# Kernel optimization log

Hardware: AMD Instinct MI355X
Metric: run time of the kernel (lower is better)

## Reference

```python
import jax, jax.numpy as jnp
import numpy as np

EPS = 1e-7
R = 3  # routing iterations


def conv(x, k, b, stride):
    y = jax.lax.conv_general_dilated(x, k, (stride, stride), 'VALID',
                                     dimension_numbers=('NHWC', 'HWIO', 'NHWC'))
    return y + b


def squash(s):
    n = jnp.linalg.norm(s, axis=-1, keepdims=True)
    return (n * n) / (1.0 + n * n) * s / (n + EPS)


def setup_inputs() -> dict:
    key = jax.random.key(0)
    ks = jax.random.split(key, 12)
    B = 256

    def g(k, shape, scale=0.05):
        return jax.random.normal(k, shape, dtype=jnp.float32) * scale

    return dict(
        x=jax.random.normal(ks[0], (B, 40, 40, 1), dtype=jnp.float32),
        y=jax.random.randint(ks[1], (B,), 0, 10),
        conv1_k=g(ks[2], (5, 5, 1, 64)),   conv1_b=jnp.zeros((64,), jnp.float32),
        conv2_k=g(ks[3], (9, 9, 64, 128)), conv2_b=jnp.zeros((128,), jnp.float32),
        conv3_k=g(ks[4], (9, 9, 128, 256)), conv3_b=jnp.zeros((256,), jnp.float32),
        prim_k=g(ks[5], (9, 9, 256, 256)), prim_b=jnp.zeros((256,), jnp.float32),
        w=g(ks[6], (1152, 10, 16, 8)),
        d1_w=g(ks[7], (160, 1024)),  d1_b=jnp.zeros((1024,), jnp.float32),
        d2_w=g(ks[8], (1024, 2048)), d2_b=jnp.zeros((2048,), jnp.float32),
        d3_w=g(ks[9], (2048, 1600)), d3_b=jnp.zeros((1600,), jnp.float32),
    )


def reference(x, y, conv1_k, conv1_b, conv2_k, conv2_b, conv3_k, conv3_b,
              prim_k, prim_b, w, d1_w, d1_b, d2_w, d2_b, d3_w, d3_b):
    # conv stack: 40 -> 36 -> 28 -> 20 -> 6 (primary caps, stride 2, linear)
    h = jax.nn.relu(conv(x, conv1_k, conv1_b, 1))
    h = jax.nn.relu(conv(h, conv2_k, conv2_b, 1))
    h = jax.nn.relu(conv(h, conv3_k, conv3_b, 1))
    h = conv(h, prim_k, prim_b, 2)                      # [B,6,6,256]
    B = h.shape[0]
    u = h.reshape(B, 1152, 8)                           # 1152 primary capsules of dim 8

    # pose predictions: u_hat[b,i,j,k] = sum_v w[i,j,k,v] * u[b,i,v]
    u_hat = jnp.einsum('ijkv,biv->bijk', w, u)          # [B,1152,10,16]

    # dynamic routing by agreement
    b_logit = jnp.zeros((B, 1152, 10), dtype=u_hat.dtype)
    for _ in range(R):
        c = jax.nn.softmax(b_logit, axis=2)[..., None]          # [B,1152,10,1]
        s = jnp.sum(c * u_hat, axis=1, keepdims=True)           # [B,1,10,16]
        v = squash(s)                                           # [B,1,10,16]
        b_logit = b_logit + jnp.sum(u_hat * v, axis=-1)         # agreement

    # masking by true label and reconstruction
    yh = jax.nn.one_hot(y, 10, dtype=v.dtype)                   # [B,10]
    v_masked = yh[:, None, :, None] * v                         # [B,1,10,16]
    v_flat = v_masked.reshape(B, 10 * 16)
    r1 = jax.nn.relu(v_flat @ d1_w + d1_b)
    r2 = jax.nn.relu(r1 @ d2_w + d2_b)
    recon = jax.nn.sigmoid(r2 @ d3_w + d3_b)                    # [B,1600]
    return (v, recon)
```

## Files before the change

kernel.cpp:

```cpp
#include <hip/hip_runtime.h>
#include <hip/hip_bf16.h>

typedef _Float16 f16;
typedef __attribute__((ext_vector_type(8))) _Float16 f16x8;
typedef __attribute__((ext_vector_type(4))) float f32x4;

__device__ __forceinline__ void gload_lds16(const void* g, void* l) {
  __builtin_amdgcn_global_load_lds((const __attribute__((address_space(1))) void*)g,
                                   (__attribute__((address_space(3))) void*)l, 16, 0, 0);
}

template<int CIN, int COUT>
__global__ __launch_bounds__(256) void wtrans_kernel(const float* __restrict__ src,
                                                     f16* __restrict__ dst) {
  constexpr int KT = 81 * CIN;
  __shared__ float tile[64][65];
  int k0 = blockIdx.x * 64;
  int n0 = blockIdx.y * 64;
  int t = threadIdx.x;
#pragma unroll
  for (int i = 0; i < 16; ++i) {
    int id = t + i * 256;
    int r = id >> 6, c = id & 63;
    tile[r][c] = src[(k0 + r) * COUT + n0 + c];
  }
  __syncthreads();
#pragma unroll
  for (int i = 0; i < 16; ++i) {
    int id = t + i * 256;
    int r = id >> 6, c = id & 63;
    dst[(n0 + r) * KT + k0 + c] = (f16)tile[c][r];
  }
}

__global__ __launch_bounds__(256) void wtransg_kernel(const float* __restrict__ src,
                                                      f16* __restrict__ dst,
                                                      int K, int N, int NP) {
  __shared__ float tile[64][65];
  int k0 = blockIdx.x * 64;
  int n0 = blockIdx.y * 64;
  int t = threadIdx.x;
#pragma unroll
  for (int i = 0; i < 16; ++i) {
    int id = t + i * 256;
    int r = id >> 6, c = id & 63;
    tile[r][c] = (n0 + c < N) ? src[(k0 + r) * N + n0 + c] : 0.f;
  }
  __syncthreads();
#pragma unroll
  for (int i = 0; i < 16; ++i) {
    int id = t + i * 256;
    int r = id >> 6, c = id & 63;
    dst[(size_t)(n0 + r) * K + k0 + c] = (f16)tile[c][r];
  }
}

__global__ __launch_bounds__(256) void cvtf16_kernel(const float* __restrict__ src,
                                                     f16* __restrict__ dst, int n) {
  int idx = blockIdx.x * 256 + threadIdx.x;
  if (idx < n) dst[idx] = (f16)src[idx];
}

__global__ __launch_bounds__(256) void conv1_kernel(const float* __restrict__ x,
                                                    const float* __restrict__ kw,
                                                    const float* __restrict__ bias,
                                                    f16* __restrict__ out) {
  int idx = blockIdx.x * 256 + threadIdx.x;
  int g = idx & 7;
  int co0 = g * 8;
  int r = idx >> 3;
  int ow = r % 36; int r2 = r / 36; int oh = r2 % 36; int b = r2 / 36;
  float acc[8];
#pragma unroll
  for (int j = 0; j < 8; ++j) acc[j] = bias[co0 + j];
  const float* xp = x + (b * 40 + oh) * 40 + ow;
#pragma unroll
  for (int dy = 0; dy < 5; ++dy)
#pragma unroll
    for (int dx = 0; dx < 5; ++dx) {
      float xv = xp[dy * 40 + dx];
      const float* kp = kw + (dy * 5 + dx) * 64 + co0;
#pragma unroll
      for (int j = 0; j < 8; ++j) acc[j] += xv * kp[j];
    }
  f16x8 o;
#pragma unroll
  for (int j = 0; j < 8; ++j) o[j] = (f16)fmaxf(acc[j], 0.f);
  *(f16x8*)(out + r * 64 + co0) = o;
}

template<int CIN, int WIN>
__device__ __forceinline__ int tapA_off(int kt) {
  int tap, ci0;
  if (CIN == 64)       { tap = kt;      ci0 = 0; }
  else if (CIN == 128) { tap = kt >> 1; ci0 = (kt & 1) << 6; }
  else                 { tap = kt >> 2; ci0 = (kt & 3) << 6; }
  int dy = tap / 9, dx = tap - dy * 9;
  return (dy * WIN + dx) * CIN + ci0;
}

template<int HIN, int WIN, int CIN, int HOUT, int WOUT, int COUT, int STRIDE,
         bool RELU, bool OUTF16>
__global__ __launch_bounds__(512, 2) void conv8p_kernel(const f16* __restrict__ in,
                                                        const f16* __restrict__ wt,
                                                        const float* __restrict__ bias,
                                                        f16* __restrict__ out16,
                                                        float* __restrict__ out32) {
  static_assert(COUT == 256, "BN=256 template requires COUT==256");
  constexpr int KTOT = 81 * CIN;
  constexpr int NT = KTOT / 64;
  __shared__ __align__(16) f16 lds[65536];
  const int mb = (int)blockIdx.x;
  const int t = threadIdx.x;
  const int wave = t >> 6, lane = t & 63;
  const int hi = lane >> 4, lo = lane & 15;
  const int wm = wave >> 2, wn = wave & 3;

  int Aoff[4], Boff[4];
  {
    int g = (lane & 7) ^ ((lane >> 3) & 7);
#pragma unroll
    for (int rbi = 0; rbi < 4; ++rbi) {
      int r = rbi * 64 + 8 * wave + (lane >> 3);
      int m = mb * 256 + r;
      int b = m / (HOUT * WOUT);
      int rr = m - b * (HOUT * WOUT);
      int oh = rr / WOUT, ow = rr - oh * WOUT;
      Aoff[rbi] = ((b * HIN + oh * STRIDE) * WIN + ow * STRIDE) * CIN + g * 8;
      Boff[rbi] = r * KTOT + g * 8;
    }
  }
  const int gb0 = (hi ^ (lo & 7)) << 4;
  const int gb1 = ((4 + hi) ^ (lo & 7)) << 4;

  const char* ldsc = (const char*)lds;
  char* ldsw = (char*)lds;

#define GA(rbi, tpo, bq) gload_lds16(in + Aoff[rbi] + (tpo),                        \
    (void*)(ldsw + (bq) * 32768 + ((rbi) * 64 + 8 * wave) * 128))
#define GB(rbi, tile) gload_lds16(wt + Boff[rbi] + ((tile) << 6),                   \
    (void*)(ldsw + 65536 + ((tile) & 1) * 32768 + ((rbi) * 64 + 8 * wave) * 128))

  {
    int tp0 = tapA_off<CIN, WIN>(0);
    GA(0, tp0, 0); GA(2, tp0, 0); GA(1, tp0, 0); GA(3, tp0, 0);
    GB(0, 0); GB(1, 0); GB(2, 0); GB(3, 0);
    GB(0, 1); GB(1, 1); GB(2, 1); GB(3, 1);
    asm volatile("s_waitcnt vmcnt(4)" ::: "memory");
    __builtin_amdgcn_s_barrier();
  }

  f32x4 acc[8][4] = {};

#define DO_PHASE(Q, STAGE)                                                          \
  {                                                                                 \
    f16x8 af[2][2];                                                                 \
    _Pragma("unroll")                                                               \
    for (int mf = 0; mf < 2; ++mf) {                                                \
      af[mf][0] = *(const f16x8*)(Ab + ((Q) * 2 + mf) * 2048 + gb0);                \
      af[mf][1] = *(const f16x8*)(Ab + ((Q) * 2 + mf) * 2048 + gb1);                \
    }                                                                               \
    STAGE;                                                                          \
    __builtin_amdgcn_s_barrier();                                                   \
    asm volatile("s_waitcnt lgkmcnt(0)" ::: "memory");                              \
    __builtin_amdgcn_sched_barrier(0);                                              \
    __builtin_amdgcn_s_setprio(1);                                                  \
    _Pragma("unroll")                                                               \
    for (int sb = 0; sb < 2; ++sb)                                                  \
      _Pragma("unroll")                                                             \
      for (int mf = 0; mf < 2; ++mf)                                                \
        _Pragma("unroll")                                                           \
        for (int nf = 0; nf < 4; ++nf)                                              \
          acc[(Q) * 2 + mf][nf] = __builtin_amdgcn_mfma_f32_16x16x32_f16(           \
              af[mf][sb], bfr[nf][sb], acc[(Q) * 2 + mf][nf], 0, 0, 0);             \
    __builtin_amdgcn_s_setprio(0);                                                  \
    __builtin_amdgcn_s_barrier();                                                   \
  }

  for (int T = 0; T < NT; ++T) {
    const int q = T & 1;
    const char* Ab = ldsc + q * 32768 + wm * 16384 + lo * 128;
    const char* Bb = ldsc + 65536 + q * 32768 + wn * 8192 + lo * 128;
    const int tpn = tapA_off<CIN, WIN>(T + 1);
    f16x8 bfr[4][2];
#pragma unroll
    for (int nf = 0; nf < 4; ++nf) {
      bfr[nf][0] = *(const f16x8*)(Bb + nf * 2048 + gb0);
      bfr[nf][1] = *(const f16x8*)(Bb + nf * 2048 + gb1);
    }
    DO_PHASE(0, if (T + 1 < NT) { GA(0, tpn, (T + 1) & 1); GA(2, tpn, (T + 1) & 1); })
    DO_PHASE(1, if (T + 1 < NT) { GA(1, tpn, (T + 1) & 1); GA(3, tpn, (T + 1) & 1); })
    DO_PHASE(2, if (T + 2 < NT) { GB(0, T + 2); GB(1, T + 2); })
    DO_PHASE(3,
      if (T + 2 < NT) {
        GB(2, T + 2); GB(3, T + 2);
        asm volatile("s_waitcnt vmcnt(4)" ::: "memory");
      } else {
        asm volatile("s_waitcnt vmcnt(0)" ::: "memory");
      })
  }
#undef DO_PHASE
#undef GA
#undef GB

#pragma unroll
  for (int mfr = 0; mfr < 8; ++mfr) {
#pragma unroll
    for (int nf = 0; nf < 4; ++nf) {
      int m0 = mb * 256 + wm * 128 + mfr * 16 + hi * 4;
      int n = wn * 64 + nf * 16 + lo;
      float bval = bias[n];
#pragma unroll
      for (int r = 0; r < 4; ++r) {
        float v = acc[mfr][nf][r] + bval;
        if (RELU) v = fmaxf(v, 0.f);
        int o = (m0 + r) * COUT + n;
        if (OUTF16) out16[o] = (f16)v; else out32[o] = v;
      }
    }
  }
}

template<int HIN, int WIN, int CIN, int HOUT, int WOUT, int COUT, int STRIDE,
         bool RELU, bool OUTF16, int SPLIT, bool ADDBIAS>
__global__ __launch_bounds__(256) void conv_mfma_kernel(const f16* __restrict__ in,
                                                        const f16* __restrict__ wt,
                                                        const float* __restrict__ bias,
                                                        f16* __restrict__ out16,
                                                        float* __restrict__ out32) {
  constexpr int KTOT = 81 * CIN;
  constexpr int NBLK = COUT / 128;
  constexpr int MTOT = 256 * HOUT * WOUT;
  constexpr int MBNB = (MTOT / 128) * NBLK;
  constexpr int NKT = (KTOT / 64) / SPLIT;
  __shared__ __align__(16) f16 lds[16384];
  int bidx = (int)blockIdx.x;
  int ks = 0;
  if (SPLIT > 1) { ks = bidx / MBNB; bidx -= ks * MBNB; }
  const int mb = bidx / NBLK;
  const int nb = bidx % NBLK;
  const int t = threadIdx.x;
  const int wave = t >> 6, lane = t & 63;
  const int hi = lane >> 4, lo = lane & 15;
  const bool isA = wave < 2;
  const int slot0 = wave << 9;

  int baseoff[8];
#pragma unroll
  for (int it = 0; it < 8; ++it) {
    int s = slot0 + it * 64 + lane;
    if (isA) {
      int row = s >> 3;
      int g = (s & 7) ^ (row & 7);
      int mg = mb * 128 + row;
      int b = mg / (HOUT * WOUT);
      int rr = mg - b * (HOUT * WOUT);
      int oh = rr / WOUT;
      int ow = rr - oh * WOUT;
      baseoff[it] = ((b * HIN + oh * STRIDE) * WIN + ow * STRIDE) * CIN + g * 8;
    } else {
      int sl = s - 1024;
      int row = sl >> 3;
      int g = (sl & 7) ^ (row & 7);
      baseoff[it] = (nb * 128 + row) * KTOT + g * 8;
    }
  }
  const f16* gsrc = isA ? in : wt;

  int aQ[4], bQ[4];
  const int wm = wave >> 1, wn = wave & 1;
#pragma unroll
  for (int f = 0; f < 4; ++f) {
    int arow = wm * 64 + f * 16 + lo;
    aQ[f] = (arow * 128) ^ ((arow & 7) << 4);
    int brow = wn * 64 + f * 16 + lo;
    bQ[f] = 16384 + ((brow * 128) ^ ((brow & 7) << 4));
  }

  f32x4 acc[4][4] = {};
  const char* ldsc = (const char*)lds;

  const int kt0 = ks * NKT;
  for (int kt = kt0; kt < kt0 + NKT; ++kt) {
    int tapoff;
    if (isA) tapoff = tapA_off<CIN, WIN>(kt);
    else     tapoff = kt << 6;
    __syncthreads();
#pragma unroll
    for (int it = 0; it < 8; ++it)
      gload_lds16(gsrc + baseoff[it] + tapoff,
                  (void*)((char*)lds + ((slot0 + it * 64) << 4)));
    __syncthreads();
#pragma unroll
    for (int sub = 0; sub < 2; ++sub) {
      const int gx = (sub * 4 + hi) << 4;
      f16x8 av[4], bv[4];
#pragma unroll
      for (int f = 0; f < 4; ++f) av[f] = *(const f16x8*)(ldsc + (aQ[f] ^ gx));
#pragma unroll
      for (int f = 0; f < 4; ++f) bv[f] = *(const f16x8*)(ldsc + (bQ[f] ^ gx));
#pragma unroll
      for (int mf = 0; mf < 4; ++mf)
#pragma unroll
        for (int nf = 0; nf < 4; ++nf)
          acc[mf][nf] = __builtin_amdgcn_mfma_f32_16x16x32_f16(av[mf], bv[nf],
                                                               acc[mf][nf], 0, 0, 0);
    }
  }

  float* o32 = out32 + (size_t)ks * MTOT * COUT;
#pragma unroll
  for (int mf = 0; mf < 4; ++mf) {
#pragma unroll
    for (int nf = 0; nf < 4; ++nf) {
      int m0 = mb * 128 + wm * 64 + mf * 16 + hi * 4;
      int n = nb * 128 + wn * 64 + nf * 16 + lo;
      float bval = ADDBIAS ? bias[n] : 0.f;
#pragma unroll
      for (int r = 0; r < 4; ++r) {
        float v = acc[mf][nf][r] + bval;
        if (RELU) v = fmaxf(v, 0.f);
        int o = (m0 + r) * COUT + n;
        if (OUTF16) out16[o] = (f16)v; else o32[o] = v;
      }
    }
  }
}

__global__ __launch_bounds__(256) void prim_reduce_kernel(const float* __restrict__ part,
                                                          const float* __restrict__ bias,
                                                          float* __restrict__ p) {
  int idx = blockIdx.x * 256 + threadIdx.x;
  int n = idx & 255;
  float a = bias[n];
#pragma unroll
  for (int s = 0; s < 4; ++s) a += part[s * 2359296 + idx];
  p[idx] = a;
}

template<int K, int NP, int NOUT, int ACT>
__global__ __launch_bounds__(256) void gemm_mfma_kernel(const f16* __restrict__ A,
                                                        const f16* __restrict__ Bw,
                                                        const float* __restrict__ bias,
                                                        f16* __restrict__ out16,
                                                        float* __restrict__ out32) {
  constexpr int NBLK = NP / 128;
  __shared__ __align__(16) f16 lds[16384];
  const int mb = (int)blockIdx.x / NBLK;
  const int nb = (int)blockIdx.x % NBLK;
  const int t = threadIdx.x;
  const int wave = t >> 6, lane = t & 63;
  const int hi = lane >> 4, lo = lane & 15;
  const bool isA = wave < 2;
  const int slot0 = wave << 9;

  int baseoff[8];
#pragma unroll
  for (int it = 0; it < 8; ++it) {
    int s = slot0 + it * 64 + lane;
    if (isA) {
      int row = s >> 3;
      int g = (s & 7) ^ (row & 7);
      baseoff[it] = (mb * 128 + row) * K + g * 8;
    } else {
      int sl = s - 1024;
      int row = sl >> 3;
      int g = (sl & 7) ^ (row & 7);
      baseoff[it] = (nb * 128 + row) * K + g * 8;
    }
  }
  const f16* gsrc = isA ? A : Bw;

  int aQ[4], bQ[4];
  const int wm = wave >> 1, wn = wave & 1;
#pragma unroll
  for (int f = 0; f < 4; ++f) {
    int arow = wm * 64 + f * 16 + lo;
    aQ[f] = (arow * 128) ^ ((arow & 7) << 4);
    int brow = wn * 64 + f * 16 + lo;
    bQ[f] = 16384 + ((brow * 128) ^ ((brow & 7) << 4));
  }

  f32x4 acc[4][4] = {};
  const char* ldsc = (const char*)lds;

  for (int kt = 0; kt < K / 64; ++kt) {
    int tapoff = kt << 6;
    __syncthreads();
#pragma unroll
    for (int it = 0; it < 8; ++it)
      gload_lds16(gsrc + baseoff[it] + tapoff,
                  (void*)((char*)lds + ((slot0 + it * 64) << 4)));
    __syncthreads();
#pragma unroll
    for (int sub = 0; sub < 2; ++sub) {
      const int gx = (sub * 4 + hi) << 4;
      f16x8 av[4], bv[4];
#pragma unroll
      for (int f = 0; f < 4; ++f) av[f] = *(const f16x8*)(ldsc + (aQ[f] ^ gx));
#pragma unroll
      for (int f = 0; f < 4; ++f) bv[f] = *(const f16x8*)(ldsc + (bQ[f] ^ gx));
#pragma unroll
      for (int mf = 0; mf < 4; ++mf)
#pragma unroll
        for (int nf = 0; nf < 4; ++nf)
          acc[mf][nf] = __builtin_amdgcn_mfma_f32_16x16x32_f16(av[mf], bv[nf],
                                                               acc[mf][nf], 0, 0, 0);
    }
  }

#pragma unroll
  for (int mf = 0; mf < 4; ++mf) {
#pragma unroll
    for (int nf = 0; nf < 4; ++nf) {
      int m0 = mb * 128 + wm * 64 + mf * 16 + hi * 4;
      int n = nb * 128 + wn * 64 + nf * 16 + lo;
      if (n < NOUT) {
        float bval = bias[n];
#pragma unroll
        for (int r = 0; r < 4; ++r) {
          float v = acc[mf][nf][r] + bval;
          if (ACT == 0) out16[(m0 + r) * NOUT + n] = (f16)fmaxf(v, 0.f);
          else          out32[(m0 + r) * NOUT + n] = 1.f / (1.f + expf(-v));
        }
      }
    }
  }
}

__global__ __launch_bounds__(320) void uhatps_kernel(const f16* __restrict__ wf,
                                                     const float* __restrict__ u,
                                                     f16* __restrict__ uh,
                                                     float* __restrict__ parts) {
  __shared__ float pl[128][8];
  int blk = (int)blockIdx.x;
  int b = blk / 9, ic = blk - b * 9;
  int t = threadIdx.x;
  const float* pb = u + (b * 1152 + ic * 128) * 8;
  for (int e = t; e < 1024; e += 320) pl[e >> 3][e & 7] = pb[e];
  __syncthreads();
  int half = (t >= 160) ? 1 : 0;
  int jk = t - half * 160;
  int ibase = ic * 128 + half * 64;
  float sum = 0.f;
  for (int il = 0; il < 64; ++il) {
    int i = ibase + il;
    f16x8 wv = *(const f16x8*)(wf + (i * 160 + jk) * 8);
    const float* pr = pl[half * 64 + il];
    float acc = (float)wv[0] * pr[0] + (float)wv[1] * pr[1] + (float)wv[2] * pr[2] +
                (float)wv[3] * pr[3] + (float)wv[4] * pr[4] + (float)wv[5] * pr[5] +
                (float)wv[6] * pr[6] + (float)wv[7] * pr[7];
    uh[(b * 1152 + i) * 160 + jk] = (f16)acc;
    sum += acc;
  }
  parts[(b * 18 + ic * 2 + half) * 160 + jk] = sum;
}

__global__ __launch_bounds__(160) void sred_kernel(const float* __restrict__ parts,
                                                   float cscale, int nch,
                                                   float* __restrict__ vbuf,
                                                   float* __restrict__ vout) {
  int b = blockIdx.x, t = threadIdx.x;
  float s = 0.f;
  for (int c = 0; c < nch; ++c) s += parts[(b * nch + c) * 160 + t];
  s *= cscale;
  float ss = s * s;
  ss += __shfl_xor(ss, 1, 16);
  ss += __shfl_xor(ss, 2, 16);
  ss += __shfl_xor(ss, 4, 16);
  ss += __shfl_xor(ss, 8, 16);
  float n = sqrtf(ss);
  float f = ss / ((1.f + ss) * (n + 1e-7f));
  float v = f * s;
  vbuf[b * 160 + t] = v;
  if (vout) vout[b * 160 + t] = v;
}

template<bool FIRST, bool WRITEB>
__global__ __launch_bounds__(256) void ba_kernel(const f16* __restrict__ uh,
                                                 const float* __restrict__ vbuf,
                                                 float* __restrict__ blog,
                                                 float* __restrict__ parts) {
  __shared__ f16 ul[128 * 172];
  __shared__ float vl[160];
  __shared__ float csm[128 * 10];
  int blk = (int)blockIdx.x;
  int b = blk / 9, ic = blk - b * 9;
  int t = threadIdx.x;
  const f16* ub = uh + (size_t)(b * 1152 + ic * 128) * 160;
  for (int e = t; e < 2560; e += 256) {
    int row = e / 20, col = e - row * 20;
    *(f16x8*)(ul + row * 172 + col * 8) = *(const f16x8*)(ub + row * 160 + col * 8);
  }
  if (t < 160) vl[t] = vbuf[b * 160 + t];
  __syncthreads();

  int il = t >> 1, half = t & 1, j0 = half * 5;
  const f16* ur = ul + il * 172 + j0 * 16;
  float agr[5];
#pragma unroll
  for (int j = 0; j < 5; ++j) {
    f16x8 a0 = *(const f16x8*)(ur + j * 16);
    f16x8 a1 = *(const f16x8*)(ur + j * 16 + 8);
    const float* vv = vl + (j0 + j) * 16;
    float s = (float)a0[0] * vv[0] + (float)a0[1] * vv[1] + (float)a0[2] * vv[2] +
              (float)a0[3] * vv[3] + (float)a0[4] * vv[4] + (float)a0[5] * vv[5] +
              (float)a0[6] * vv[6] + (float)a0[7] * vv[7] +
              (float)a1[0] * vv[8] + (float)a1[1] * vv[9] + (float)a1[2] * vv[10] +
              (float)a1[3] * vv[11] + (float)a1[4] * vv[12] + (float)a1[5] * vv[13] +
              (float)a1[6] * vv[14] + (float)a1[7] * vv[15];
    agr[j] = s;
  }
  int bbase = (b * 1152 + ic * 128 + il) * 10 + j0;
  float bl[5];
#pragma unroll
  for (int j = 0; j < 5; ++j) bl[j] = (FIRST ? 0.f : blog[bbase + j]) + agr[j];
  if (WRITEB) {
#pragma unroll
    for (int j = 0; j < 5; ++j) blog[bbase + j] = bl[j];
  }
  float mx = bl[0];
#pragma unroll
  for (int j = 1; j < 5; ++j) mx = fmaxf(mx, bl[j]);
  mx = fmaxf(mx, __shfl_xor(mx, 1));
  float e5[5], se = 0.f;
#pragma unroll
  for (int j = 0; j < 5; ++j) { e5[j] = expf(bl[j] - mx); se += e5[j]; }
  se += __shfl_xor(se, 1);
  float inv = 1.f / se;
#pragma unroll
  for (int j = 0; j < 5; ++j) csm[il * 10 + j0 + j] = e5[j] * inv;
  __syncthreads();

  if (t < 160) {
    int j = t >> 4;
    float s = 0.f;
    for (int il2 = 0; il2 < 128; ++il2)
      s += csm[il2 * 10 + j] * (float)ul[il2 * 172 + t];
    parts[(b * 9 + ic) * 160 + t] = s;
  }
}

__global__ __launch_bounds__(256) void maskd1_kernel(const float* __restrict__ vbuf,
                                                     const int* __restrict__ y,
                                                     const float* __restrict__ w1,
                                                     const float* __restrict__ b1,
                                                     f16* __restrict__ r1) {
  int idx = blockIdx.x * 256 + threadIdx.x;
  int o = idx & 1023;
  int b = idx >> 10;
  int yb = y[b];
  const float* vv = vbuf + b * 160 + yb * 16;
  float acc = b1[o];
#pragma unroll
  for (int k = 0; k < 16; ++k) acc += vv[k] * w1[(yb * 16 + k) * 1024 + o];
  r1[idx] = (f16)fmaxf(acc, 0.f);
}

extern "C" void kernel_launch(void* const* d_in, const int* in_sizes, int n_in,
                              void* d_out, int out_size, void* d_ws, size_t ws_size,
                              hipStream_t stream) {
  const float* x       = (const float*)d_in[0];
  const int*   y       = (const int*)d_in[1];
  const float* conv1_k = (const float*)d_in[2];
  const float* conv1_b = (const float*)d_in[3];
  const float* conv2_k = (const float*)d_in[4];
  const float* conv2_b = (const float*)d_in[5];
  const float* conv3_k = (const float*)d_in[6];
  const float* conv3_b = (const float*)d_in[7];
  const float* prim_k  = (const float*)d_in[8];
  const float* prim_b  = (const float*)d_in[9];
  const float* w_route = (const float*)d_in[10];
  const float* d1_w = (const float*)d_in[11];
  const float* d1_b = (const float*)d_in[12];
  const float* d2_w = (const float*)d_in[13];
  const float* d2_b = (const float*)d_in[14];
  const float* d3_w = (const float*)d_in[15];
  const float* d3_b = (const float*)d_in[16];

  char* ws = (char*)d_ws;
  f16*   h1    = (f16*)(ws + 0);
  f16*   h2    = (f16*)(ws + 42467328);
  f16*   h3    = (f16*)(ws + 93847552);
  float* part  = (float*)(ws + 0);
  f16*   uhat  = (f16*)(ws + 0);
  float* parts = (float*)(ws + 94371840);
  float* p     = (float*)(ws + 146276352);
  float* blog  = (float*)(ws + 155713536);
  f16*   wd2   = (f16*)(ws + 155713536);
  f16*   wd3   = (f16*)(ws + 159907840);
  float* vbuf  = (float*)(ws + 167510016);
  f16*   r1h   = (f16*)(ws + 167673856);
  f16*   r2h   = (f16*)(ws + 168198144);
  f16*   wt2   = (f16*)(ws + 170819584);
  f16*   wt3   = (f16*)(ws + 172146688);
  f16*   wtp   = (f16*)(ws + 177455104);
  f16*   wf16  = (f16*)(ws + 188071936);

  float* vout  = (float*)d_out;
  float* recon = (float*)d_out + 40960;

  wtrans_kernel<64, 128><<<dim3(81, 2), 256, 0, stream>>>(conv2_k, wt2);
  wtrans_kernel<128, 256><<<dim3(162, 4), 256, 0, stream>>>(conv3_k, wt3);
  wtrans_kernel<256, 256><<<dim3(324, 4), 256, 0, stream>>>(prim_k, wtp);
  cvtf16_kernel<<<5760, 256, 0, stream>>>(w_route, wf16, 1474560);

  conv1_kernel<<<10368, 256, 0, stream>>>(x, conv1_k, conv1_b, h1);
  conv_mfma_kernel<36, 36, 64, 28, 28, 128, 1, true, true, 1, true>
      <<<1568, 256, 0, stream>>>(h1, wt2, conv2_b, h2, nullptr);
  conv8p_kernel<28, 28, 128, 20, 20, 256, 1, true, true>
      <<<400, 512, 0, stream>>>(h2, wt3, conv3_b, h3, nullptr);
  conv_mfma_kernel<20, 20, 256, 6, 6, 256, 2, false, false, 4, false>
      <<<576, 256, 0, stream>>>(h3, wtp, prim_b, nullptr, part);
  prim_reduce_kernel<<<9216, 256, 0, stream>>>(part, prim_b, p);

  uhatps_kernel<<<2304, 320, 0, stream>>>(wf16, p, uhat, parts);
  sred_kernel<<<256, 160, 0, stream>>>(parts, 0.1f, 18, vbuf, nullptr);
  ba_kernel<true, true><<<2304, 256, 0, stream>>>(uhat, vbuf, blog, parts);
  sred_kernel<<<256, 160, 0, stream>>>(parts, 1.0f, 9, vbuf, nullptr);
  ba_kernel<false, false><<<2304, 256, 0, stream>>>(uhat, vbuf, blog, parts);
  sred_kernel<<<256, 160, 0, stream>>>(parts, 1.0f, 9, vbuf, vout);

  wtransg_kernel<<<dim3(16, 32), 256, 0, stream>>>(d2_w, wd2, 1024, 2048, 2048);
  wtransg_kernel<<<dim3(32, 26), 256, 0, stream>>>(d3_w, wd3, 2048, 1600, 1664);
  maskd1_kernel<<<1024, 256, 0, stream>>>(vbuf, y, d1_w, d1_b, r1h);
  gemm_mfma_kernel<1024, 2048, 2048, 0><<<32, 256, 0, stream>>>(r1h, wd2, d2_b, r2h, nullptr);
  gemm_mfma_kernel<2048, 1664, 1600, 1><<<26, 256, 0, stream>>>(r2h, wd3, d3_b, nullptr, recon);
}
```

Baseline: 1.257 ms.

## Split-K the decoder GEMMs and read fp32 routing weights directly

The two decoder GEMMs previously ran on only 32 and 26 workgroups. They now use split-K across 4 and 8 slices, writing fp32 partial sums that separate reduce kernels combine while applying bias, ReLU or sigmoid. This fills more of the GPU's compute units at the cost of extra partial-sum traffic and two extra launches. Separately, the fp16 conversion kernel for the routing weights is removed and uhatps reads the fp32 weights directly, saving one launch but doubling the bytes that kernel reads.

```diff
diff --git a/kernel.cpp b/kernel.cpp
--- a/kernel.cpp
+++ b/kernel.cpp
@@ -53,12 +53,6 @@
     int r = id >> 6, c = id & 63;
     dst[(size_t)(n0 + r) * K + k0 + c] = (f16)tile[c][r];
   }
-}
-
-__global__ __launch_bounds__(256) void cvtf16_kernel(const float* __restrict__ src,
-                                                     f16* __restrict__ dst, int n) {
-  int idx = blockIdx.x * 256 + threadIdx.x;
-  if (idx < n) dst[idx] = (f16)src[idx];
 }
 
 __global__ __launch_bounds__(256) void conv1_kernel(const float* __restrict__ x,
@@ -338,16 +332,19 @@
   p[idx] = a;
 }
 
-template<int K, int NP, int NOUT, int ACT>
+template<int K, int NP, int SPLIT>
 __global__ __launch_bounds__(256) void gemm_mfma_kernel(const f16* __restrict__ A,
                                                         const f16* __restrict__ Bw,
-                                                        const float* __restrict__ bias,
-                                                        f16* __restrict__ out16,
-                                                        float* __restrict__ out32) {
+                                                        float* __restrict__ dpart) {
   constexpr int NBLK = NP / 128;
+  constexpr int MBNB = 2 * NBLK;
+  constexpr int NKT = (K / 64) / SPLIT;
   __shared__ __align__(16) f16 lds[16384];
-  const int mb = (int)blockIdx.x / NBLK;
-  const int nb = (int)blockIdx.x % NBLK;
+  int bidx = (int)blockIdx.x;
+  int ks = 0;
+  if (SPLIT > 1) { ks = bidx / MBNB; bidx -= ks * MBNB; }
+  const int mb = bidx / NBLK;
+  const int nb = bidx % NBLK;
   const int t = threadIdx.x;
   const int wave = t >> 6, lane = t & 63;
   const int hi = lane >> 4, lo = lane & 15;
@@ -384,7 +381,8 @@
   f32x4 acc[4][4] = {};
   const char* ldsc = (const char*)lds;
 
-  for (int kt = 0; kt < K / 64; ++kt) {
+  const int kt0 = ks * NKT;
+  for (int kt = kt0; kt < kt0 + NKT; ++kt) {
     int tapoff = kt << 6;
     __syncthreads();
 #pragma unroll
@@ -409,26 +407,59 @@
     }
   }
 
+  float* o32 = dpart + (size_t)ks * 256 * NP;
 #pragma unroll
   for (int mf = 0; mf < 4; ++mf) {
 #pragma unroll
     for (int nf = 0; nf < 4; ++nf) {
       int m0 = mb * 128 + wm * 64 + mf * 16 + hi * 4;
       int n = nb * 128 + wn * 64 + nf * 16 + lo;
-      if (n < NOUT) {
-        float bval = bias[n];
-#pragma unroll
-        for (int r = 0; r < 4; ++r) {
-          float v = acc[mf][nf][r] + bval;
-          if (ACT == 0) out16[(m0 + r) * NOUT + n] = (f16)fmaxf(v, 0.f);
-          else          out32[(m0 + r) * NOUT + n] = 1.f / (1.f + expf(-v));
-        }
-      }
-    }
-  }
-}
-
-__global__ __launch_bounds__(320) void uhatps_kernel(const f16* __restrict__ wf,
+#pragma unroll
+      for (int r = 0; r < 4; ++r)
+        o32[(m0 + r) * NP + n] = acc[mf][nf][r];
+    }
+  }
+}
+
+__global__ __launch_bounds__(256) void d2red_kernel(const float* __restrict__ part,
+                                                    const float* __restrict__ bias,
+                                                    f16* __restrict__ r2) {
+  int idx = blockIdx.x * 256 + threadIdx.x;
+  int e0 = idx * 4;
+  int n0 = e0 & 2047;
+  float4 a = *(const float4*)(part + e0);
+  const float4 b1 = *(const float4*)(part + 524288 + e0);
+  const float4 b2 = *(const float4*)(part + 1048576 + e0);
+  const float4 b3 = *(const float4*)(part + 1572864 + e0);
+  float v[4] = {a.x + b1.x + b2.x + b3.x, a.y + b1.y + b2.y + b3.y,
+                a.z + b1.z + b2.z + b3.z, a.w + b1.w + b2.w + b3.w};
+#pragma unroll
+  for (int j = 0; j < 4; ++j)
+    r2[e0 + j] = (f16)fmaxf(v[j] + bias[n0 + j], 0.f);
+}
+
+__global__ __launch_bounds__(256) void d3red_kernel(const float* __restrict__ part,
+                                                    const float* __restrict__ bias,
+                                                    float* __restrict__ recon) {
+  int idx = blockIdx.x * 256 + threadIdx.x;
+  int e0 = idx * 4;
+  int n0 = e0 % 1664;
+  int m = e0 / 1664;
+  float v[4] = {0.f, 0.f, 0.f, 0.f};
+#pragma unroll
+  for (int s = 0; s < 8; ++s) {
+    float4 a = *(const float4*)(part + s * 425984 + e0);
+    v[0] += a.x; v[1] += a.y; v[2] += a.z; v[3] += a.w;
+  }
+#pragma unroll
+  for (int j = 0; j < 4; ++j) {
+    int n = n0 + j;
+    if (n < 1600)
+      recon[m * 1600 + n] = 1.f / (1.f + expf(-(v[j] + bias[n])));
+  }
+}
+
+__global__ __launch_bounds__(320) void uhatps_kernel(const float* __restrict__ wf,
                                                      const float* __restrict__ u,
                                                      f16* __restrict__ uh,
                                                      float* __restrict__ parts) {
@@ -445,11 +476,11 @@
   float sum = 0.f;
   for (int il = 0; il < 64; ++il) {
     int i = ibase + il;
-    f16x8 wv = *(const f16x8*)(wf + (i * 160 + jk) * 8);
+    const float4* w4 = (const float4*)(wf + (i * 160 + jk) * 8);
+    float4 w0 = w4[0], w1 = w4[1];
     const float* pr = pl[half * 64 + il];
-    float acc = (float)wv[0] * pr[0] + (float)wv[1] * pr[1] + (float)wv[2] * pr[2] +
-                (float)wv[3] * pr[3] + (float)wv[4] * pr[4] + (float)wv[5] * pr[5] +
-                (float)wv[6] * pr[6] + (float)wv[7] * pr[7];
+    float acc = w0.x * pr[0] + w0.y * pr[1] + w0.z * pr[2] + w0.w * pr[3] +
+                w1.x * pr[4] + w1.y * pr[5] + w1.z * pr[6] + w1.w * pr[7];
     uh[(b * 1152 + i) * 160 + jk] = (f16)acc;
     sum += acc;
   }
@@ -579,23 +610,24 @@
   const float* d3_b = (const float*)d_in[16];
 
   char* ws = (char*)d_ws;
-  f16*   h1    = (f16*)(ws + 0);
-  f16*   h2    = (f16*)(ws + 42467328);
-  f16*   h3    = (f16*)(ws + 93847552);
-  float* part  = (float*)(ws + 0);
-  f16*   uhat  = (f16*)(ws + 0);
-  float* parts = (float*)(ws + 94371840);
-  float* p     = (float*)(ws + 146276352);
-  float* blog  = (float*)(ws + 155713536);
-  f16*   wd2   = (f16*)(ws + 155713536);
-  f16*   wd3   = (f16*)(ws + 159907840);
-  float* vbuf  = (float*)(ws + 167510016);
-  f16*   r1h   = (f16*)(ws + 167673856);
-  f16*   r2h   = (f16*)(ws + 168198144);
-  f16*   wt2   = (f16*)(ws + 170819584);
-  f16*   wt3   = (f16*)(ws + 172146688);
-  f16*   wtp   = (f16*)(ws + 177455104);
-  f16*   wf16  = (f16*)(ws + 188071936);
+  f16*   h1     = (f16*)(ws + 0);
+  f16*   h2     = (f16*)(ws + 42467328);
+  f16*   h3     = (f16*)(ws + 93847552);
+  float* part   = (float*)(ws + 0);
+  f16*   uhat   = (f16*)(ws + 0);
+  float* dpart2 = (float*)(ws + 0);
+  float* dpart3 = (float*)(ws + 16777216);
+  float* parts  = (float*)(ws + 94371840);
+  float* p      = (float*)(ws + 146276352);
+  float* blog   = (float*)(ws + 155713536);
+  f16*   wd2    = (f16*)(ws + 155713536);
+  f16*   wd3    = (f16*)(ws + 159907840);
+  float* vbuf   = (float*)(ws + 167510016);
+  f16*   r1h    = (f16*)(ws + 167673856);
+  f16*   r2h    = (f16*)(ws + 168198144);
+  f16*   wt2    = (f16*)(ws + 170819584);
+  f16*   wt3    = (f16*)(ws + 172146688);
+  f16*   wtp    = (f16*)(ws + 177455104);
 
   float* vout  = (float*)d_out;
   float* recon = (float*)d_out + 40960;
@@ -603,7 +635,6 @@
   wtrans_kernel<64, 128><<<dim3(81, 2), 256, 0, stream>>>(conv2_k, wt2);
   wtrans_kernel<128, 256><<<dim3(162, 4), 256, 0, stream>>>(conv3_k, wt3);
   wtrans_kernel<256, 256><<<dim3(324, 4), 256, 0, stream>>>(prim_k, wtp);
-  cvtf16_kernel<<<5760, 256, 0, stream>>>(w_route, wf16, 1474560);
 
   conv1_kernel<<<10368, 256, 0, stream>>>(x, conv1_k, conv1_b, h1);
   conv_mfma_kernel<36, 36, 64, 28, 28, 128, 1, true, true, 1, true>
@@ -614,7 +645,7 @@
       <<<576, 256, 0, stream>>>(h3, wtp, prim_b, nullptr, part);
   prim_reduce_kernel<<<9216, 256, 0, stream>>>(part, prim_b, p);
 
-  uhatps_kernel<<<2304, 320, 0, stream>>>(wf16, p, uhat, parts);
+  uhatps_kernel<<<2304, 320, 0, stream>>>(w_route, p, uhat, parts);
   sred_kernel<<<256, 160, 0, stream>>>(parts, 0.1f, 18, vbuf, nullptr);
   ba_kernel<true, true><<<2304, 256, 0, stream>>>(uhat, vbuf, blog, parts);
   sred_kernel<<<256, 160, 0, stream>>>(parts, 1.0f, 9, vbuf, nullptr);
@@ -624,6 +655,8 @@
   wtransg_kernel<<<dim3(16, 32), 256, 0, stream>>>(d2_w, wd2, 1024, 2048, 2048);
   wtransg_kernel<<<dim3(32, 26), 256, 0, stream>>>(d3_w, wd3, 2048, 1600, 1664);
   maskd1_kernel<<<1024, 256, 0, stream>>>(vbuf, y, d1_w, d1_b, r1h);
-  gemm_mfma_kernel<1024, 2048, 2048, 0><<<32, 256, 0, stream>>>(r1h, wd2, d2_b, r2h, nullptr);
-  gemm_mfma_kernel<2048, 1664, 1600, 1><<<26, 256, 0, stream>>>(r2h, wd3, d3_b, nullptr, recon);
-}
+  gemm_mfma_kernel<1024, 2048, 4><<<128, 256, 0, stream>>>(r1h, wd2, dpart2);
+  d2red_kernel<<<512, 256, 0, stream>>>(dpart2, d2_b, r2h);
+  gemm_mfma_kernel<2048, 1664, 8><<<208, 256, 0, stream>>>(r2h, wd3, dpart3);
+  d3red_kernel<<<416, 256, 0, stream>>>(dpart3, d3_b, recon);
+}
```

Measured after the change: 1.259 ms. Within noise of the previous version (+0.1%).
